# Kernel tuning notes

Hardware: AMD Instinct MI355X
Metric: run time of the kernel (lower is better)

The kernel has to match this reference:

```python
import jax, jax.numpy as jnp
import numpy as np

H = 2048          # hidden_size
F = 1408          # moe_intermediate_size
E = 64            # n_routed_experts
TOP_K = 6         # num_experts_per_tok
CAP = 512         # per-expert capacity (mean load ~192; overflow prob ~0)
SCALE = 1.0       # routed_scaling_factor
F_SH = 2 * F      # shared-expert intermediate (n_shared_experts=2)
B, S = 1, 2048


def setup_inputs() -> dict:
    key = jax.random.key(0)
    ks = jax.random.split(key, 8)
    s = 0.02
    return {
        "hidden_states": jax.random.normal(ks[0], (B, S, H), jnp.float32),
        "gate_w":  jax.random.normal(ks[1], (E, H), jnp.float32) * s,
        "w_gate":  jax.random.normal(ks[2], (E, H, F), jnp.float32) * s,
        "w_up":    jax.random.normal(ks[3], (E, H, F), jnp.float32) * s,
        "w_down":  jax.random.normal(ks[4], (E, F, H), jnp.float32) * s,
        "sh_gate": jax.random.normal(ks[5], (F_SH, H), jnp.float32) * s,
        "sh_up":   jax.random.normal(ks[6], (F_SH, H), jnp.float32) * s,
        "sh_down": jax.random.normal(ks[7], (H, F_SH), jnp.float32) * s,
    }


def reference(hidden_states, gate_w, w_gate, w_up, w_down, sh_gate, sh_up, sh_down):
    b, s, _ = hidden_states.shape
    x = hidden_states.reshape(-1, H)                       # [T, H]
    T = x.shape[0]

    # ---- gate: fp32 logits -> softmax -> top-k, scaled ----
    logits = x.astype(jnp.float32) @ gate_w.astype(jnp.float32).T   # [T, E]
    scores = jax.nn.softmax(logits, axis=-1)
    topk_w, topk_idx = jax.lax.top_k(scores, TOP_K)        # [T, K] (order irrelevant: summed)
    topk_w = topk_w * SCALE

    # ---- dispatch: sort expanded tokens by expert, scatter into [E, CAP, H] ----
    eid = topk_idx.reshape(-1)                             # [T*K]
    x_exp = jnp.repeat(x, TOP_K, axis=0)                   # [T*K, H] (token t repeated K times)
    order = jnp.argsort(eid)                               # stable sort by expert id
    eid_s = eid[order]
    counts = jnp.bincount(eid, length=E)
    starts = jnp.cumsum(counts) - counts                   # exclusive prefix sums
    pos = jnp.arange(T * TOP_K) - starts[eid_s]            # slot within expert
    valid = pos < CAP
    pos_c = jnp.where(valid, pos, CAP)                     # overflow -> scratch slot CAP
    buf = jnp.zeros((E, CAP + 1, H), x.dtype).at[eid_s, pos_c].set(x_exp[order])

    # ---- grouped expert SwiGLU MLP (grouped GEMM as batched einsum) ----
    g = jax.nn.silu(jnp.einsum('ech,ehf->ecf', buf, w_gate))
    u = jnp.einsum('ech,ehf->ecf', buf, w_up)
    d = jnp.einsum('ecf,efh->ech', g * u, w_down)          # [E, CAP+1, H]

    # ---- combine: gather, unsort, weighted sum over top-k ----
    out_s = jnp.where(valid[:, None], d[eid_s, pos_c], 0.0)
    out_exp = jnp.zeros_like(out_s).at[order].set(out_s)   # reverse_shuffle
    y = jnp.einsum('tkh,tk->th', out_exp.reshape(T, TOP_K, H), topk_w)
    y = y.astype(x.dtype).reshape(b, s, H)

    # ---- shared experts residual (dense SwiGLU MLP on identity) ----
    gs = jax.nn.silu(hidden_states @ sh_gate.T)
    us = hidden_states @ sh_up.T
    y = y + (gs * us) @ sh_down.T
    return y
```

## Files before the change

### kernel.cpp

```cpp
#include <hip/hip_runtime.h>
#include <hip/hip_bf16.h>

#define H 2048
#define FDIM 1408
#define NE 64
#define CAP 512
#define NTOK 2048
#define FSH 2816

typedef float  f32x4  __attribute__((ext_vector_type(4)));
typedef short  s16x8  __attribute__((ext_vector_type(8)));
typedef unsigned short u16;
typedef u16    u16x4v __attribute__((ext_vector_type(4)));

__device__ __forceinline__ u16 f2bf(float f) {
    union { float f; unsigned u; } v; v.f = f;
    unsigned u = v.u;
    u += 0x7fffu + ((u >> 16) & 1u);
    return (u16)(u >> 16);
}
__device__ __forceinline__ float bf2f(u16 b) {
    union { unsigned u; float f; } v; v.u = ((unsigned)b) << 16;
    return v.f;
}
__device__ __forceinline__ int swze(int row) {
    return (((row & 7) ^ ((row >> 3) & 7)) << 3);
}
__device__ __forceinline__ void wr4(u16* dst, float a, float b, float c, float d) {
    u16x4v v; v[0] = f2bf(a); v[1] = f2bf(b); v[2] = f2bf(c); v[3] = f2bf(d);
    *(u16x4v*)dst = v;
}
__device__ __forceinline__ void glds16(const u16* g, u16* l) {
    __builtin_amdgcn_global_load_lds(
        (const __attribute__((address_space(1))) unsigned int*)g,
        (__attribute__((address_space(3))) unsigned int*)l, 16, 0, 0);
}

#define BAR() do { asm volatile("s_waitcnt lgkmcnt(0)" ::: "memory"); \
                   __builtin_amdgcn_s_barrier(); } while (0)
#define WAIT_VM(N)  asm volatile("s_waitcnt vmcnt(" #N ")" ::: "memory")
#define SCHED_FENCE() __builtin_amdgcn_sched_barrier(0)

__global__ __launch_bounds__(256) void xcvt(const float* __restrict__ x, u16* __restrict__ xb) {
    int i = blockIdx.x * 256 + threadIdx.x;
    const float4 a = ((const float4*)x)[2 * i];
    const float4 b = ((const float4*)x)[2 * i + 1];
    u16 v[8] = { f2bf(a.x), f2bf(a.y), f2bf(a.z), f2bf(a.w),
                 f2bf(b.x), f2bf(b.y), f2bf(b.z), f2bf(b.w) };
    *(s16x8*)(xb + (size_t)i * 8) = *(s16x8*)v;
}

__global__ void init_cnt(int* __restrict__ c) { c[threadIdx.x] = 0; }

__global__ __launch_bounds__(64) void gate_topk(
    const float* __restrict__ xg, const float* __restrict__ gw,
    int* __restrict__ cnt, int* __restrict__ tok_of,
    int* __restrict__ slot_enc, float* __restrict__ tw)
{
    const int t = blockIdx.x;
    const int lane = threadIdx.x;
    __shared__ float4 xs[512];
    const float4* xr = (const float4*)(xg + (size_t)t * H);
    #pragma unroll
    for (int i = 0; i < 8; ++i) xs[i * 64 + lane] = xr[i * 64 + lane];
    __syncthreads();

    const float4* gr = (const float4*)(gw + (size_t)lane * H);
    float acc = 0.f;
    #pragma unroll 4
    for (int i = 0; i < 512; ++i) {
        float4 a = xs[i], b = gr[i];
        acc += a.x * b.x + a.y * b.y + a.z * b.z + a.w * b.w;
    }
    float m = acc;
    #pragma unroll
    for (int off = 32; off; off >>= 1) m = fmaxf(m, __shfl_xor(m, off));
    float p = __expf(acc - m);
    float s = p;
    #pragma unroll
    for (int off = 32; off; off >>= 1) s += __shfl_xor(s, off);
    p = p / s;

    float myw = 0.f; int mye = 0;
    float v = p;
    for (int k = 0; k < 6; ++k) {
        float bv = v; int bi = lane;
        #pragma unroll
        for (int off = 32; off; off >>= 1) {
            float ov = __shfl_xor(bv, off);
            int   oi = __shfl_xor(bi, off);
            if (ov > bv || (ov == bv && oi < bi)) { bv = ov; bi = oi; }
        }
        if (lane == k)  { myw = bv; mye = bi; }
        if (lane == bi) v = -1.f;
    }
    if (lane < 6) {
        int slot = atomicAdd(&cnt[mye], 1);
        int enc = -1;
        if (slot < CAP) { tok_of[mye * CAP + slot] = t; enc = mye * CAP + slot; }
        slot_enc[t * 6 + lane] = enc;
        tw[t * 6 + lane] = myw;
    }
}

template<bool ROUTED>
__global__ __launch_bounds__(256, 2) void dual_gemm(
    const u16* __restrict__ xbf, const int* __restrict__ tok_of,
    const int* __restrict__ cnt_arr, const float* __restrict__ wg,
    const float* __restrict__ wu, u16* __restrict__ act, int Fd)
{
    __shared__ u16 As[2][256 * 64];
    __shared__ u16 Bgs[32 * 64];
    __shared__ u16 Bus[32 * 64];

    int e = 0, cnt, m0, f0;
    if constexpr (ROUTED) {
        e = blockIdx.z;
        cnt = cnt_arr[e]; cnt = cnt < CAP ? cnt : CAP;
        f0 = blockIdx.x * 32; m0 = blockIdx.y * 256;
        if (m0 >= cnt) return;
    } else {
        cnt = NTOK;
        m0 = blockIdx.x * 256; f0 = blockIdx.y * 32;
    }

    const float* wg_e = wg;
    const float* wu_e = wu;
    u16* act_e = act;
    if constexpr (ROUTED) {
        wg_e += (size_t)e * H * Fd;
        wu_e += (size_t)e * H * Fd;
        act_e += (size_t)e * CAP * Fd;
    }

    const int tid = threadIdx.x;
    const int lane = tid & 63;
    const int wv = tid >> 6;
    const int NT = H / 64;

    const u16* agp[8];
    #pragma unroll
    for (int it = 0; it < 8; ++it) {
        int rloc = it * 32 + wv * 8 + (lane >> 3);
        int srow = m0 + rloc;
        int gcol = (((lane & 7) ^ (lane >> 3) ^ ((it * 4 + wv) & 7)) << 3);
        const u16* base;
        if constexpr (ROUTED) {
            const int* tok = tok_of + e * CAP;
            base = xbf + (size_t)tok[srow < cnt ? srow : 0] * H;
        } else {
            base = xbf + (size_t)srow * H;
        }
        agp[it] = base + gcol;
    }
    const int mat = tid >> 7;
    const int bb = tid & 127;
    const float* bsrc;
    int bn4 = 0, bkb = 0, br = 0, bc = 0;
    if constexpr (ROUTED) {
        bn4 = bb & 7; bkb = bb >> 3;
        bsrc = (mat ? wu_e : wg_e) + (size_t)(bkb * 4) * Fd + f0 + bn4 * 4;
    } else {
        br = bb >> 2; bc = bb & 3;
        bsrc = (mat ? wu_e : wg_e) + (size_t)(f0 + br) * H + bc * 16;
    }

    f32x4 accg[4][2], accu[4][2];
    const f32x4 zero4 = {0.f, 0.f, 0.f, 0.f};
    #pragma unroll
    for (int i = 0; i < 4; ++i)
        #pragma unroll
        for (int j = 0; j < 2; ++j) { accg[i][j] = zero4; accu[i][j] = zero4; }

    f32x4 bR[4];

    auto GLDS_A = [&](int kt, int b) {
        #pragma unroll
        for (int it = 0; it < 8; ++it)
            glds16(agp[it] + kt * 64, &As[b][(it * 32 + wv * 8) * 64]);
    };
    auto LOADB = [&](int kt) {
        if constexpr (ROUTED) {
            #pragma unroll
            for (int j = 0; j < 4; ++j)
                bR[j] = *(const f32x4*)(bsrc + ((size_t)kt * 64 + j) * Fd);
        } else {
            #pragma unroll
            for (int q = 0; q < 4; ++q)
                bR[q] = *(const f32x4*)(bsrc + kt * 64 + q * 4);
        }
    };
    auto STOREB = [&]() {
        u16* Bdst = mat ? Bus : Bgs;
        if constexpr (ROUTED) {
            #pragma unroll
            for (int j = 0; j < 4; ++j) {
                int rr = bn4 * 4 + j;
                wr4(&Bdst[rr * 64 + ((bkb * 4) ^ swze(rr))],
                    bR[0][j], bR[1][j], bR[2][j], bR[3][j]);
            }
        } else {
            #pragma unroll
            for (int q = 0; q < 4; ++q)
                wr4(&Bdst[br * 64 + ((bc * 16 + q * 4) ^ swze(br))],
                    bR[q].x, bR[q].y, bR[q].z, bR[q].w);
        }
    };
    auto COMPUTE = [&](int b) {
        __builtin_amdgcn_s_setprio(1);
        #pragma unroll
        for (int kk = 0; kk < 2; ++kk) {
            const int ko = kk * 32 + (lane >> 4) * 8;
            s16x8 a[4], bg[2], bu[2];
            #pragma unroll
            for (int mi = 0; mi < 4; ++mi) {
                int r = wv * 64 + mi * 16 + (lane & 15);
                a[mi] = *(const s16x8*)&As[b][r * 64 + (ko ^ swze(r))];
            }
            #pragma unroll
            for (int ni = 0; ni < 2; ++ni) {
                int r = ni * 16 + (lane & 15);
                bg[ni] = *(const s16x8*)&Bgs[r * 64 + (ko ^ swze(r))];
                bu[ni] = *(const s16x8*)&Bus[r * 64 + (ko ^ swze(r))];
            }
            #pragma unroll
            for (int mi = 0; mi < 4; ++mi)
                #pragma unroll
                for (int ni = 0; ni < 2; ++ni) {
                    accg[mi][ni] = __builtin_amdgcn_mfma_f32_16x16x32_bf16(a[mi], bg[ni], accg[mi][ni], 0, 0, 0);
                    accu[mi][ni] = __builtin_amdgcn_mfma_f32_16x16x32_bf16(a[mi], bu[ni], accu[mi][ni], 0, 0, 0);
                }
        }
        __builtin_amdgcn_s_setprio(0);
    };

    GLDS_A(0, 0); SCHED_FENCE();
    LOADB(0);     SCHED_FENCE();
    STOREB();
    LOADB(1);     SCHED_FENCE();
    WAIT_VM(4);
    BAR(); SCHED_FENCE();

    for (int kt = 0; kt < NT; ++kt) {
        const int b = kt & 1;
        if (kt + 1 < NT) GLDS_A(kt + 1, b ^ 1);
        SCHED_FENCE();
        COMPUTE(b);
        BAR();
        if (kt + 1 < NT) {
            STOREB();
            if (kt + 2 < NT) LOADB(kt + 2);
        }
        SCHED_FENCE();
        if (kt + 1 < NT) {
            if (kt + 2 < NT) { WAIT_VM(4); }
            else             { WAIT_VM(0); }
        }
        BAR(); SCHED_FENCE();
    }

    #pragma unroll
    for (int mi = 0; mi < 4; ++mi)
        #pragma unroll
        for (int ni = 0; ni < 2; ++ni)
            #pragma unroll
            for (int r = 0; r < 4; ++r) {
                int srow = m0 + wv * 64 + mi * 16 + (lane >> 4) * 4 + r;
                if (srow < cnt) {
                    int fc = f0 + ni * 16 + (lane & 15);
                    float g = accg[mi][ni][r], u = accu[mi][ni][r];
                    float aa = (g / (1.f + __expf(-g))) * u;
                    act_e[(size_t)srow * Fd + fc] = f2bf(aa);
                }
            }
}

template<bool ROUTED>
__global__ __launch_bounds__(256, 2) void down_gemm(
    const u16* __restrict__ actA, const float* __restrict__ wdn,
    void* __restrict__ outp, const int* __restrict__ cnt_arr, int Kd)
{
    __shared__ u16 As[2][256 * 64];
    __shared__ u16 Bs[64 * 64];

    int e = 0, cnt, m0, n0;
    if constexpr (ROUTED) {
        e = blockIdx.z;
        cnt = cnt_arr[e]; cnt = cnt < CAP ? cnt : CAP;
        n0 = blockIdx.x * 64; m0 = blockIdx.y * 256;
        if (m0 >= cnt) return;
    } else {
        cnt = NTOK;
        m0 = blockIdx.x * 256; n0 = blockIdx.y * 64;
    }

    const u16* A_e = actA;
    const float* B_e = wdn;
    if constexpr (ROUTED) {
        A_e += (size_t)e * CAP * Kd;
        B_e += (size_t)e * Kd * H;
    }
    const int NT = Kd / 64;
    const int tid = threadIdx.x, lane = tid & 63, wv = tid >> 6;

    const u16* agp[8];
    #pragma unroll
    for (int it = 0; it < 8; ++it) {
        int rloc = it * 32 + wv * 8 + (lane >> 3);
        int gcol = (((lane & 7) ^ (lane >> 3) ^ ((it * 4 + wv) & 7)) << 3);
        agp[it] = A_e + (size_t)(m0 + rloc) * Kd + gcol;
    }
    const float* bsrc;
    int bn4 = 0, bkq = 0, dr = 0, dc = 0;
    if constexpr (ROUTED) {
        bn4 = tid & 15; bkq = tid >> 4;
        bsrc = B_e + (size_t)(bkq * 4) * H + n0 + bn4 * 4;
    } else {
        dr = tid >> 2; dc = tid & 3;
        bsrc = B_e + (size_t)(n0 + dr) * FSH + dc * 16;
    }

    f32x4 acc[4][4];
    const f32x4 zero4 = {0.f, 0.f, 0.f, 0.f};
    #pragma unroll
    for (int i = 0; i < 4; ++i)
        #pragma unroll
        for (int j = 0; j < 4; ++j) acc[i][j] = zero4;

    f32x4 bR[4];

    auto GLDS_A = [&](int kt, int b) {
        #pragma unroll
        for (int it = 0; it < 8; ++it)
            glds16(agp[it] + kt * 64, &As[b][(it * 32 + wv * 8) * 64]);
    };
    auto LOADB = [&](int kt) {
        if constexpr (ROUTED) {
            #pragma unroll
            for (int j = 0; j < 4; ++j)
                bR[j] = *(const f32x4*)(bsrc + ((size_t)kt * 64 + j) * H);
        } else {
            #pragma unroll
            for (int q = 0; q < 4; ++q)
                bR[q] = *(const f32x4*)(bsrc + kt * 64 + q * 4);
        }
    };
    auto STOREB = [&]() {
        if constexpr (ROUTED) {
            #pragma unroll
            for (int j = 0; j < 4; ++j) {
                int rr = bn4 * 4 + j;
                wr4(&Bs[rr * 64 + ((bkq * 4) ^ swze(rr))],
                    bR[0][j], bR[1][j], bR[2][j], bR[3][j]);
            }
        } else {
            #pragma unroll
            for (int q = 0; q < 4; ++q)
                wr4(&Bs[dr * 64 + ((dc * 16 + q * 4) ^ swze(dr))],
                    bR[q].x, bR[q].y, bR[q].z, bR[q].w);
        }
    };
    auto COMPUTE = [&](int b) {
        __builtin_amdgcn_s_setprio(1);
        #pragma unroll
        for (int kk = 0; kk < 2; ++kk) {
            const int ko = kk * 32 + (lane >> 4) * 8;
            s16x8 a[4], bf[4];
            #pragma unroll
            for (int mi = 0; mi < 4; ++mi) {
                int r = wv * 64 + mi * 16 + (lane & 15);
                a[mi] = *(const s16x8*)&As[b][r * 64 + (ko ^ swze(r))];
            }
            #pragma unroll
            for (int ni = 0; ni < 4; ++ni) {
                int r = ni * 16 + (lane & 15);
                bf[ni] = *(const s16x8*)&Bs[r * 64 + (ko ^ swze(r))];
            }
            #pragma unroll
            for (int mi = 0; mi < 4; ++mi)
                #pragma unroll
                for (int ni = 0; ni < 4; ++ni)
                    acc[mi][ni] = __builtin_amdgcn_mfma_f32_16x16x32_bf16(a[mi], bf[ni], acc[mi][ni], 0, 0, 0);
        }
        __builtin_amdgcn_s_setprio(0);
    };

    GLDS_A(0, 0); SCHED_FENCE();
    LOADB(0);     SCHED_FENCE();
    STOREB();
    LOADB(1);     SCHED_FENCE();
    WAIT_VM(4);
    BAR(); SCHED_FENCE();

    for (int kt = 0; kt < NT; ++kt) {
        const int b = kt & 1;
        if (kt + 1 < NT) GLDS_A(kt + 1, b ^ 1);
        SCHED_FENCE();
        COMPUTE(b);
        BAR();
        if (kt + 1 < NT) {
            STOREB();
            if (kt + 2 < NT) LOADB(kt + 2);
        }
        SCHED_FENCE();
        if (kt + 1 < NT) {
            if (kt + 2 < NT) { WAIT_VM(4); }
            else             { WAIT_VM(0); }
        }
        BAR(); SCHED_FENCE();
    }

    #pragma unroll
    for (int mi = 0; mi < 4; ++mi)
        #pragma unroll
        for (int ni = 0; ni < 4; ++ni)
            #pragma unroll
            for (int r = 0; r < 4; ++r) {
                int srow = m0 + wv * 64 + mi * 16 + (lane >> 4) * 4 + r;
                if (srow < cnt) {
                    int col = n0 + ni * 16 + (lane & 15);
                    float vv = acc[mi][ni][r];
                    if constexpr (ROUTED)
                        ((u16*)outp)[(size_t)e * CAP * H + (size_t)srow * H + col] = f2bf(vv);
                    else
                        ((float*)outp)[(size_t)srow * H + col] = vv;
                }
            }
}

__global__ __launch_bounds__(256) void combine(
    float* __restrict__ y, const u16* __restrict__ d,
    const int* __restrict__ slot_enc, const float* __restrict__ tw)
{
    const int t = blockIdx.x, tid = threadIdx.x;
    int enc[6]; float w[6];
    #pragma unroll
    for (int k = 0; k < 6; ++k) {
        enc[k] = slot_enc[t * 6 + k];
        w[k] = tw[t * 6 + k];
    }
    float4* yrow = (float4*)(y + (size_t)t * H);
    #pragma unroll
    for (int it = 0; it < 2; ++it) {
        int h4 = it * 256 + tid;
        float4 acc = yrow[h4];
        #pragma unroll
        for (int k = 0; k < 6; ++k) {
            if (enc[k] >= 0) {
                ushort4 dv = ((const ushort4*)(d + (size_t)enc[k] * H))[h4];
                acc.x += w[k] * bf2f(dv.x);
                acc.y += w[k] * bf2f(dv.y);
                acc.z += w[k] * bf2f(dv.z);
                acc.w += w[k] * bf2f(dv.w);
            }
        }
        yrow[h4] = acc;
    }
}

extern "C" void kernel_launch(void* const* d_in, const int* in_sizes, int n_in,
                              void* d_out, int out_size, void* d_ws, size_t ws_size,
                              hipStream_t stream) {
    const float* x       = (const float*)d_in[0];
    const float* gw      = (const float*)d_in[1];
    const float* w_gate  = (const float*)d_in[2];
    const float* w_up    = (const float*)d_in[3];
    const float* w_down  = (const float*)d_in[4];
    const float* sh_gate = (const float*)d_in[5];
    const float* sh_up   = (const float*)d_in[6];
    const float* sh_down = (const float*)d_in[7];
    float* y = (float*)d_out;

    char* wsb = (char*)d_ws;
    int*   cnt      = (int*)(wsb + 0);
    int*   tok_of   = (int*)(wsb + 512);
    int*   slot_enc = (int*)(wsb + 512 + 131072);
    float* tw       = (float*)(wsb + 512 + 131072 + 49152);
    u16*   act      = (u16*)(wsb + 230144);
    u16*   actsh    = (u16*)(wsb + 230144 + 92274688);
    u16*   dbuf     = (u16*)(wsb + 230144 + 92274688 + 11534336);
    u16*   xbf      = dbuf;

    init_cnt<<<1, 64, 0, stream>>>(cnt);
    xcvt<<<NTOK * H / 8 / 256, 256, 0, stream>>>(x, xbf);
    gate_topk<<<NTOK, 64, 0, stream>>>(x, gw, cnt, tok_of, slot_enc, tw);
    dual_gemm<true><<<dim3(FDIM / 32, 2, NE), 256, 0, stream>>>(
        xbf, tok_of, cnt, w_gate, w_up, act, FDIM);
    dual_gemm<false><<<dim3(NTOK / 256, FSH / 32, 1), 256, 0, stream>>>(
        xbf, nullptr, nullptr, sh_gate, sh_up, actsh, FSH);
    down_gemm<true><<<dim3(H / 64, 2, NE), 256, 0, stream>>>(
        act, w_down, (void*)dbuf, cnt, FDIM);
    down_gemm<false><<<dim3(NTOK / 256, H / 64, 1), 256, 0, stream>>>(
        actsh, sh_down, (void*)y, nullptr, FSH);
    combine<<<NTOK, 256, 0, stream>>>(y, dbuf, slot_enc, tw);
}
```

Measured before the change: 998.1 us.

## Halve K-tile to 32 with new LDS layouts to fit three blocks per CU

Cuts the K step of the dual and down GEMMs from 64 to 32, shrinking shared-memory tiles, and raises launch bounds to allow three blocks per CU. It replaces the row-XOR swizzled B layout with a k-chunk-major layout and a new 4-way swizzle for A, rewriting the loaders and MFMA fragment reads to match. The aim is more occupancy to hide the fp32 weight-load latency. In exchange it doubles the number of barriers and loop iterations per output tile, and register pressure under the tighter launch bound may cause spills. It also removes the initial vmcnt wait before the first barrier, which may race.

```diff
diff --git a/kernel.cpp b/kernel.cpp
--- a/kernel.cpp
+++ b/kernel.cpp
@@ -9,6 +9,7 @@
 #define FSH 2816
 
 typedef float  f32x4  __attribute__((ext_vector_type(4)));
+typedef float  f32x2  __attribute__((ext_vector_type(2)));
 typedef short  s16x8  __attribute__((ext_vector_type(8)));
 typedef unsigned short u16;
 typedef u16    u16x4v __attribute__((ext_vector_type(4)));
@@ -22,13 +23,6 @@
 __device__ __forceinline__ float bf2f(u16 b) {
     union { unsigned u; float f; } v; v.u = ((unsigned)b) << 16;
     return v.f;
-}
-__device__ __forceinline__ int swze(int row) {
-    return (((row & 7) ^ ((row >> 3) & 7)) << 3);
-}
-__device__ __forceinline__ void wr4(u16* dst, float a, float b, float c, float d) {
-    u16x4v v; v[0] = f2bf(a); v[1] = f2bf(b); v[2] = f2bf(c); v[3] = f2bf(d);
-    *(u16x4v*)dst = v;
 }
 __device__ __forceinline__ void glds16(const u16* g, u16* l) {
     __builtin_amdgcn_global_load_lds(
@@ -104,14 +98,14 @@
 }
 
 template<bool ROUTED>
-__global__ __launch_bounds__(256, 2) void dual_gemm(
+__global__ __launch_bounds__(256, 3) void dual_gemm(
     const u16* __restrict__ xbf, const int* __restrict__ tok_of,
     const int* __restrict__ cnt_arr, const float* __restrict__ wg,
     const float* __restrict__ wu, u16* __restrict__ act, int Fd)
 {
-    __shared__ u16 As[2][256 * 64];
-    __shared__ u16 Bgs[32 * 64];
-    __shared__ u16 Bus[32 * 64];
+    __shared__ u16 As[2][256 * 32];
+    __shared__ u16 Bgs[4 * 32 * 8];
+    __shared__ u16 Bus[4 * 32 * 8];
 
     int e = 0, cnt, m0, f0;
     if constexpr (ROUTED) {
@@ -136,14 +130,14 @@
     const int tid = threadIdx.x;
     const int lane = tid & 63;
     const int wv = tid >> 6;
-    const int NT = H / 64;
-
-    const u16* agp[8];
-    #pragma unroll
-    for (int it = 0; it < 8; ++it) {
-        int rloc = it * 32 + wv * 8 + (lane >> 3);
+    const int NT = H / 32;
+
+    const int gA = ((lane & 3) ^ ((lane >> 3) & 3)) * 8;
+    const u16* agp[4];
+    #pragma unroll
+    for (int q = 0; q < 4; ++q) {
+        int rloc = (q * 4 + wv) * 16 + (lane >> 2);
         int srow = m0 + rloc;
-        int gcol = (((lane & 7) ^ (lane >> 3) ^ ((it * 4 + wv) & 7)) << 3);
         const u16* base;
         if constexpr (ROUTED) {
             const int* tok = tok_of + e * CAP;
@@ -151,18 +145,18 @@
         } else {
             base = xbf + (size_t)srow * H;
         }
-        agp[it] = base + gcol;
+        agp[q] = base + gA;
     }
     const int mat = tid >> 7;
     const int bb = tid & 127;
     const float* bsrc;
-    int bn4 = 0, bkb = 0, br = 0, bc = 0;
-    if constexpr (ROUTED) {
-        bn4 = bb & 7; bkb = bb >> 3;
-        bsrc = (mat ? wu_e : wg_e) + (size_t)(bkb * 4) * Fd + f0 + bn4 * 4;
+    int n2 = 0, kq = 0, dr = 0, dcq = 0;
+    if constexpr (ROUTED) {
+        n2 = bb & 15; kq = bb >> 4;
+        bsrc = (mat ? wu_e : wg_e) + (size_t)(kq * 4) * Fd + f0 + n2 * 2;
     } else {
-        br = bb >> 2; bc = bb & 3;
-        bsrc = (mat ? wu_e : wg_e) + (size_t)(f0 + br) * H + bc * 16;
+        dr = bb >> 2; dcq = bb & 3;
+        bsrc = (mat ? wu_e : wg_e) + (size_t)(f0 + dr) * H + dcq * 8;
     }
 
     f32x4 accg[4][2], accu[4][2];
@@ -172,65 +166,63 @@
         #pragma unroll
         for (int j = 0; j < 2; ++j) { accg[i][j] = zero4; accu[i][j] = zero4; }
 
-    f32x4 bR[4];
+    f32x2 bR2[4];
+    f32x4 bR4[2];
 
     auto GLDS_A = [&](int kt, int b) {
         #pragma unroll
-        for (int it = 0; it < 8; ++it)
-            glds16(agp[it] + kt * 64, &As[b][(it * 32 + wv * 8) * 64]);
+        for (int q = 0; q < 4; ++q)
+            glds16(agp[q] + kt * 32, &As[b][(q * 4 + wv) * 512]);
     };
     auto LOADB = [&](int kt) {
         if constexpr (ROUTED) {
             #pragma unroll
             for (int j = 0; j < 4; ++j)
-                bR[j] = *(const f32x4*)(bsrc + ((size_t)kt * 64 + j) * Fd);
+                bR2[j] = *(const f32x2*)(bsrc + ((size_t)kt * 32 + j) * Fd);
         } else {
-            #pragma unroll
-            for (int q = 0; q < 4; ++q)
-                bR[q] = *(const f32x4*)(bsrc + kt * 64 + q * 4);
+            bR4[0] = *(const f32x4*)(bsrc + kt * 32);
+            bR4[1] = *(const f32x4*)(bsrc + kt * 32 + 4);
         }
     };
     auto STOREB = [&]() {
         u16* Bdst = mat ? Bus : Bgs;
         if constexpr (ROUTED) {
             #pragma unroll
-            for (int j = 0; j < 4; ++j) {
-                int rr = bn4 * 4 + j;
-                wr4(&Bdst[rr * 64 + ((bkb * 4) ^ swze(rr))],
-                    bR[0][j], bR[1][j], bR[2][j], bR[3][j]);
+            for (int c = 0; c < 2; ++c) {
+                u16x4v v; v[0] = f2bf(bR2[0][c]); v[1] = f2bf(bR2[1][c]);
+                          v[2] = f2bf(bR2[2][c]); v[3] = f2bf(bR2[3][c]);
+                *(u16x4v*)&Bdst[(kq >> 1) * 256 + (n2 * 2 + c) * 8 + (kq & 1) * 4] = v;
             }
         } else {
-            #pragma unroll
-            for (int q = 0; q < 4; ++q)
-                wr4(&Bdst[br * 64 + ((bc * 16 + q * 4) ^ swze(br))],
-                    bR[q].x, bR[q].y, bR[q].z, bR[q].w);
+            u16 v[8];
+            v[0]=f2bf(bR4[0][0]); v[1]=f2bf(bR4[0][1]); v[2]=f2bf(bR4[0][2]); v[3]=f2bf(bR4[0][3]);
+            v[4]=f2bf(bR4[1][0]); v[5]=f2bf(bR4[1][1]); v[6]=f2bf(bR4[1][2]); v[7]=f2bf(bR4[1][3]);
+            *(s16x8*)&Bdst[dcq * 256 + dr * 8] = *(s16x8*)v;
         }
     };
     auto COMPUTE = [&](int b) {
         __builtin_amdgcn_s_setprio(1);
-        #pragma unroll
-        for (int kk = 0; kk < 2; ++kk) {
-            const int ko = kk * 32 + (lane >> 4) * 8;
-            s16x8 a[4], bg[2], bu[2];
-            #pragma unroll
-            for (int mi = 0; mi < 4; ++mi) {
-                int r = wv * 64 + mi * 16 + (lane & 15);
-                a[mi] = *(const s16x8*)&As[b][r * 64 + (ko ^ swze(r))];
-            }
+        const int j8 = lane >> 4;
+        const int p8 = (j8 ^ ((lane >> 1) & 3)) * 8;
+        s16x8 a[4], bg[2], bu[2];
+        #pragma unroll
+        for (int mi = 0; mi < 4; ++mi) {
+            int r = wv * 64 + mi * 16 + (lane & 15);
+            a[mi] = *(const s16x8*)&As[b][r * 32 + p8];
+        }
+        #pragma unroll
+        for (int ni = 0; ni < 2; ++ni) {
+            int c = ni * 16 + (lane & 15);
+            bg[ni] = *(const s16x8*)&Bgs[j8 * 256 + c * 8];
+            bu[ni] = *(const s16x8*)&Bus[j8 * 256 + c * 8];
+        }
+        #pragma unroll
+        for (int mi = 0; mi < 4; ++mi)
             #pragma unroll
             for (int ni = 0; ni < 2; ++ni) {
-                int r = ni * 16 + (lane & 15);
-                bg[ni] = *(const s16x8*)&Bgs[r * 64 + (ko ^ swze(r))];
-                bu[ni] = *(const s16x8*)&Bus[r * 64 + (ko ^ swze(r))];
-            }
-            #pragma unroll
-            for (int mi = 0; mi < 4; ++mi)
-                #pragma unroll
-                for (int ni = 0; ni < 2; ++ni) {
-                    accg[mi][ni] = __builtin_amdgcn_mfma_f32_16x16x32_bf16(a[mi], bg[ni], accg[mi][ni], 0, 0, 0);
-                    accu[mi][ni] = __builtin_amdgcn_mfma_f32_16x16x32_bf16(a[mi], bu[ni], accu[mi][ni], 0, 0, 0);
-                }
-        }
+                accg[mi][ni] = __builtin_amdgcn_mfma_f32_16x16x32_bf16(a[mi], bg[ni], accg[mi][ni], 0, 0, 0);
+                accu[mi][ni] = __builtin_amdgcn_mfma_f32_16x16x32_bf16(a[mi], bu[ni], accu[mi][ni], 0, 0, 0);
+            }
         __builtin_amdgcn_s_setprio(0);
     };
 
@@ -238,7 +230,6 @@
     LOADB(0);     SCHED_FENCE();
     STOREB();
     LOADB(1);     SCHED_FENCE();
-    WAIT_VM(4);
     BAR(); SCHED_FENCE();
 
     for (int kt = 0; kt < NT; ++kt) {
@@ -253,8 +244,9 @@
         }
         SCHED_FENCE();
         if (kt + 1 < NT) {
-            if (kt + 2 < NT) { WAIT_VM(4); }
-            else             { WAIT_VM(0); }
+            if (kt + 2 < NT) {
+                if constexpr (ROUTED) { WAIT_VM(4); } else { WAIT_VM(2); }
+            } else { WAIT_VM(0); }
         }
         BAR(); SCHED_FENCE();
     }
@@ -276,12 +268,12 @@
 }
 
 template<bool ROUTED>
-__global__ __launch_bounds__(256, 2) void down_gemm(
+__global__ __launch_bounds__(256, 3) void down_gemm(
     const u16* __restrict__ actA, const float* __restrict__ wdn,
     void* __restrict__ outp, const int* __restrict__ cnt_arr, int Kd)
 {
-    __shared__ u16 As[2][256 * 64];
-    __shared__ u16 Bs[64 * 64];
+    __shared__ u16 As[2][256 * 32];
+    __shared__ u16 Bs[4 * 64 * 8];
 
     int e = 0, cnt, m0, n0;
     if constexpr (ROUTED) {
@@ -300,24 +292,24 @@
         A_e += (size_t)e * CAP * Kd;
         B_e += (size_t)e * Kd * H;
     }
-    const int NT = Kd / 64;
+    const int NT = Kd / 32;
     const int tid = threadIdx.x, lane = tid & 63, wv = tid >> 6;
 
-    const u16* agp[8];
-    #pragma unroll
-    for (int it = 0; it < 8; ++it) {
-        int rloc = it * 32 + wv * 8 + (lane >> 3);
-        int gcol = (((lane & 7) ^ (lane >> 3) ^ ((it * 4 + wv) & 7)) << 3);
-        agp[it] = A_e + (size_t)(m0 + rloc) * Kd + gcol;
+    const int gA = ((lane & 3) ^ ((lane >> 3) & 3)) * 8;
+    const u16* agp[4];
+    #pragma unroll
+    for (int q = 0; q < 4; ++q) {
+        int rloc = (q * 4 + wv) * 16 + (lane >> 2);
+        agp[q] = A_e + (size_t)(m0 + rloc) * Kd + gA;
     }
     const float* bsrc;
-    int bn4 = 0, bkq = 0, dr = 0, dc = 0;
-    if constexpr (ROUTED) {
-        bn4 = tid & 15; bkq = tid >> 4;
-        bsrc = B_e + (size_t)(bkq * 4) * H + n0 + bn4 * 4;
+    int n2 = 0, kq = 0, dr = 0, dcq = 0;
+    if constexpr (ROUTED) {
+        n2 = tid & 31; kq = tid >> 5;
+        bsrc = B_e + (size_t)(kq * 4) * H + n0 + n2 * 2;
     } else {
-        dr = tid >> 2; dc = tid & 3;
-        bsrc = B_e + (size_t)(n0 + dr) * FSH + dc * 16;
+        dr = tid >> 2; dcq = tid & 3;
+        bsrc = B_e + (size_t)(n0 + dr) * FSH + dcq * 8;
     }
 
     f32x4 acc[4][4];
@@ -327,61 +319,59 @@
         #pragma unroll
         for (int j = 0; j < 4; ++j) acc[i][j] = zero4;
 
-    f32x4 bR[4];
+    f32x2 bR2[4];
+    f32x4 bR4[2];
 
     auto GLDS_A = [&](int kt, int b) {
         #pragma unroll
-        for (int it = 0; it < 8; ++it)
-            glds16(agp[it] + kt * 64, &As[b][(it * 32 + wv * 8) * 64]);
+        for (int q = 0; q < 4; ++q)
+            glds16(agp[q] + kt * 32, &As[b][(q * 4 + wv) * 512]);
     };
     auto LOADB = [&](int kt) {
         if constexpr (ROUTED) {
             #pragma unroll
             for (int j = 0; j < 4; ++j)
-                bR[j] = *(const f32x4*)(bsrc + ((size_t)kt * 64 + j) * H);
+                bR2[j] = *(const f32x2*)(bsrc + ((size_t)kt * 32 + j) * H);
         } else {
-            #pragma unroll
-            for (int q = 0; q < 4; ++q)
-                bR[q] = *(const f32x4*)(bsrc + kt * 64 + q * 4);
+            bR4[0] = *(const f32x4*)(bsrc + kt * 32);
+            bR4[1] = *(const f32x4*)(bsrc + kt * 32 + 4);
         }
     };
     auto STOREB = [&]() {
         if constexpr (ROUTED) {
             #pragma unroll
-            for (int j = 0; j < 4; ++j) {
-                int rr = bn4 * 4 + j;
-                wr4(&Bs[rr * 64 + ((bkq * 4) ^ swze(rr))],
-                    bR[0][j], bR[1][j], bR[2][j], bR[3][j]);
+            for (int c = 0; c < 2; ++c) {
+                u16x4v v; v[0] = f2bf(bR2[0][c]); v[1] = f2bf(bR2[1][c]);
+                          v[2] = f2bf(bR2[2][c]); v[3] = f2bf(bR2[3][c]);
+                *(u16x4v*)&Bs[(kq >> 1) * 512 + (n2 * 2 + c) * 8 + (kq & 1) * 4] = v;
             }
         } else {
-            #pragma unroll
-            for (int q = 0; q < 4; ++q)
-                wr4(&Bs[dr * 64 + ((dc * 16 + q * 4) ^ swze(dr))],
-                    bR[q].x, bR[q].y, bR[q].z, bR[q].w);
+            u16 v[8];
+            v[0]=f2bf(bR4[0][0]); v[1]=f2bf(bR4[0][1]); v[2]=f2bf(bR4[0][2]); v[3]=f2bf(bR4[0][3]);
+            v[4]=f2bf(bR4[1][0]); v[5]=f2bf(bR4[1][1]); v[6]=f2bf(bR4[1][2]); v[7]=f2bf(bR4[1][3]);
+            *(s16x8*)&Bs[dcq * 512 + dr * 8] = *(s16x8*)v;
         }
     };
     auto COMPUTE = [&](int b) {
         __builtin_amdgcn_s_setprio(1);
-        #pragma unroll
-        for (int kk = 0; kk < 2; ++kk) {
-            const int ko = kk * 32 + (lane >> 4) * 8;
-            s16x8 a[4], bf[4];
-            #pragma unroll
-            for (int mi = 0; mi < 4; ++mi) {
-                int r = wv * 64 + mi * 16 + (lane & 15);
-                a[mi] = *(const s16x8*)&As[b][r * 64 + (ko ^ swze(r))];
-            }
-            #pragma unroll
-            for (int ni = 0; ni < 4; ++ni) {
-                int r = ni * 16 + (lane & 15);
-                bf[ni] = *(const s16x8*)&Bs[r * 64 + (ko ^ swze(r))];
-            }
-            #pragma unroll
-            for (int mi = 0; mi < 4; ++mi)
-                #pragma unroll
-                for (int ni = 0; ni < 4; ++ni)
-                    acc[mi][ni] = __builtin_amdgcn_mfma_f32_16x16x32_bf16(a[mi], bf[ni], acc[mi][ni], 0, 0, 0);
-        }
+        const int j8 = lane >> 4;
+        const int p8 = (j8 ^ ((lane >> 1) & 3)) * 8;
+        s16x8 a[4], bf[4];
+        #pragma unroll
+        for (int mi = 0; mi < 4; ++mi) {
+            int r = wv * 64 + mi * 16 + (lane & 15);
+            a[mi] = *(const s16x8*)&As[b][r * 32 + p8];
+        }
+        #pragma unroll
+        for (int ni = 0; ni < 4; ++ni) {
+            int c = ni * 16 + (lane & 15);
+            bf[ni] = *(const s16x8*)&Bs[j8 * 512 + c * 8];
+        }
+        #pragma unroll
+        for (int mi = 0; mi < 4; ++mi)
+            #pragma unroll
+            for (int ni = 0; ni < 4; ++ni)
+                acc[mi][ni] = __builtin_amdgcn_mfma_f32_16x16x32_bf16(a[mi], bf[ni], acc[mi][ni], 0, 0, 0);
         __builtin_amdgcn_s_setprio(0);
     };
 
@@ -389,7 +379,6 @@
     LOADB(0);     SCHED_FENCE();
     STOREB();
     LOADB(1);     SCHED_FENCE();
-    WAIT_VM(4);
     BAR(); SCHED_FENCE();
 
     for (int kt = 0; kt < NT; ++kt) {
@@ -404,8 +393,9 @@
         }
         SCHED_FENCE();
         if (kt + 1 < NT) {
-            if (kt + 2 < NT) { WAIT_VM(4); }
-            else             { WAIT_VM(0); }
+            if (kt + 2 < NT) {
+                if constexpr (ROUTED) { WAIT_VM(4); } else { WAIT_VM(2); }
+            } else { WAIT_VM(0); }
         }
         BAR(); SCHED_FENCE();
     }
```

Result: slower. 1.110 ms (+11.2%).
